# Kernel tuning notes

Hardware: AMD Instinct MI355X
Metric: run time of the kernel (lower is better)

The kernel has to match this reference:

```python
import jax, jax.numpy as jnp
import numpy as np

DIM = 128
HEADS = 4
WIN = 7
N = WIN * WIN  # 49 tokens per window
B = 64         # images
BDIM = 64      # windows per image (56/7)^2
B_ = B * BDIM  # 4096 total windows
HEAD_DIM = DIM // HEADS
SCALE = HEAD_DIM ** (-0.5)


def _rel_index():
    ch, cw = np.meshgrid(np.arange(WIN), np.arange(WIN), indexing='ij')
    coords = np.stack([ch.ravel(), cw.ravel()])            # [2, N]
    rel = coords[:, :, None] - coords[:, None, :]          # [2, N, N]
    rel = rel.transpose(1, 2, 0).astype(np.int32)
    rel[:, :, 0] += WIN - 1
    rel[:, :, 1] += WIN - 1
    rel[:, :, 0] *= 2 * WIN - 1
    return jnp.asarray(rel.sum(-1))                        # [N, N] in [0, 169)


def setup_inputs() -> dict:
    key = jax.random.key(0)
    ks = jax.random.split(key, 7)
    return {
        'x': jax.random.normal(ks[0], (B_, N, DIM), jnp.float32),
        'q_global': jax.random.normal(ks[1], (B, 1, HEADS, N, HEAD_DIM), jnp.float32),
        'rel_bias_table': jax.random.normal(ks[2], (169, HEADS), jnp.float32) * 0.02,
        'W_kv': jax.random.normal(ks[3], (DIM, 2 * DIM), jnp.float32) / np.sqrt(DIM),
        'b_kv': jnp.zeros((2 * DIM,), jnp.float32),
        'W_proj': jax.random.normal(ks[4], (DIM, DIM), jnp.float32) / np.sqrt(DIM),
        'b_proj': jnp.zeros((DIM,), jnp.float32),
        'rel_index': _rel_index(),
    }


def reference(x, q_global, rel_bias_table, W_kv, b_kv, W_proj, b_proj, rel_index):
    Bw, n, C = x.shape
    Bg = q_global.shape[0]
    bdim = Bw // Bg
    # kv projection: [B_, N, 2, H, hd] -> k, v each [B_, H, N, hd]
    kv = (x @ W_kv + b_kv).reshape(Bw, n, 2, HEADS, HEAD_DIM)
    kv = kv.transpose(2, 0, 3, 1, 4)
    k, v = kv[0], kv[1]
    # broadcast global q over windows of each image
    q = jnp.broadcast_to(q_global, (Bg, bdim, HEADS, n, HEAD_DIM)).reshape(Bw, HEADS, n, HEAD_DIM)
    attn = jnp.einsum('bhnd,bhmd->bhnm', q * SCALE, k)
    bias = rel_bias_table[rel_index]                        # [N, N, H]
    attn = attn + bias.transpose(2, 0, 1)[None]
    attn = jax.nn.softmax(attn, axis=-1)
    out = jnp.einsum('bhnm,bhmd->bhnd', attn, v)
    out = out.transpose(0, 2, 1, 3).reshape(Bw, n, C)
    return out @ W_proj + b_proj
```

## Files before the change

kernel.cpp:

```cpp
#include <hip/hip_runtime.h>

#define SCALE 0.17677669529663687f

typedef __attribute__((ext_vector_type(8))) short bf16x8;
typedef __attribute__((ext_vector_type(4))) short bf16x4;
typedef __attribute__((ext_vector_type(4))) float f32x4;

__device__ inline short cvt_bf16(float f) {
    union { float f; unsigned u; } v; v.f = f;
    unsigned r = v.u + 0x7fffu + ((v.u >> 16) & 1u);
    return (short)(r >> 16);
}
__device__ inline short cvt_bf16_fast(float f) {
    union { float f; unsigned u; } v; v.f = f;
    return (short)((v.u + 0x8000u) >> 16);
}
__device__ inline unsigned pack_bf16x2(float f0, float f1) {
    union { float f; unsigned u; } a, b; a.f = f0; b.f = f1;
    return __builtin_amdgcn_perm(b.u + 0x8000u, a.u + 0x8000u, 0x07060302u);
}

#if __has_builtin(__builtin_amdgcn_mfma_f32_16x16x16bf16_1k)
__device__ inline f32x4 mfma16x16(bf16x4 a, bf16x4 b, f32x4 c) {
    return __builtin_amdgcn_mfma_f32_16x16x16bf16_1k(a, b, c, 0, 0, 0);
}
#else
__device__ inline f32x4 mfma16x16(bf16x4 a, bf16x4 b, f32x4 c) {
    asm("v_mfma_f32_16x16x16_bf16 %0, %1, %2, %0" : "+v"(c) : "v"(a), "v"(b));
    return c;
}
#endif

#define WS_WPT  32768
#define WS_QW   49152
#define WS_BIAS 450560

__global__ void prep_kernel(const float* __restrict__ qg,
                            const float* __restrict__ rbt,
                            const float* __restrict__ wkv,
                            const float* __restrict__ wpj,
                            const int*   __restrict__ ridx,
                            short* __restrict__ ws) {
    int i = blockIdx.x * 256 + threadIdx.x;
    if (i < 32768) {
        int k = i >> 8, c = i & 255;
        ws[c * 128 + k] = cvt_bf16(wkv[i]);
        return;
    }
    i -= 32768;
    if (i < 16384) {
        int k = i >> 7, c = i & 127;
        ws[WS_WPT + c * 128 + k] = cvt_bf16(wpj[i]);
        return;
    }
    i -= 16384;
    if (i < 100352) {
        float4 q4 = *(const float4*)(qg + (long)i * 4);
        unsigned lo = (unsigned)(unsigned short)cvt_bf16(q4.x * SCALE) |
                      ((unsigned)(unsigned short)cvt_bf16(q4.y * SCALE) << 16);
        unsigned hi = (unsigned)(unsigned short)cvt_bf16(q4.z * SCALE) |
                      ((unsigned)(unsigned short)cvt_bf16(q4.w * SCALE) << 16);
        uint2 u; u.x = lo; u.y = hi;
        *(uint2*)(ws + WS_QW + (long)i * 4) = u;
        return;
    }
    i -= 100352;
    if (i < 12544) {
        int h = i / 3136, rem = i % 3136, ir = rem >> 6, j = rem & 63;
        float* bias = (float*)(ws + WS_BIAS);
        bias[i] = (j < 49) ? rbt[ridx[ir * 49 + j] * 4 + h] : -3.0e38f;
    }
}

#define KOFF    6664
#define KSLOT   1960
#define SMEM_SZ 14504

__global__ __launch_bounds__(256, 4) void win_attn_kernel(
        const float* __restrict__ x,
        const short* __restrict__ ws,
        const float* __restrict__ bkv,
        const float* __restrict__ bpj,
        float* __restrict__ out) {
    const int b    = blockIdx.x;
    const int img  = b >> 6;
    const int tid  = threadIdx.x;
    const int w    = tid >> 6;
    const int lane = tid & 63;
    const int quad = lane >> 4;
    const int l16  = lane & 15;

    const short* wkvt  = ws;
    const short* wpt   = ws + WS_WPT;
    const short* qw    = ws + WS_QW;
    const float* biasb = (const float*)(ws + WS_BIAS);

    __shared__ __align__(16) short smem[SMEM_SZ];
    short* xs = smem;
    short* os = smem;

    const f32x4 fzero = {0.f, 0.f, 0.f, 0.f};
    const int h = w;

    const float* xb = x + (long)b * 49 * 128;
    #pragma unroll
    for (int it = 0; it < 4; ++it) {
        int chunk = tid + it * 256;
        if (chunk < 784) {
            int row = chunk >> 4, c8 = (chunk & 15) * 8;
            const float* p = xb + row * 128 + c8;
            float4 a = *(const float4*)p;
            float4 c = *(const float4*)(p + 4);
            union { uint4 u; bf16x8 v; } pk;
            pk.u.x = pack_bf16x2(a.x, a.y);
            pk.u.y = pack_bf16x2(a.z, a.w);
            pk.u.z = pack_bf16x2(c.x, c.y);
            pk.u.w = pack_bf16x2(c.z, c.w);
            *(bf16x8*)(xs + row * 136 + c8) = pk.v;
        }
    }
    bf16x8 bfrk[4][2];
    #pragma unroll
    for (int kk = 0; kk < 4; ++kk)
        #pragma unroll
        for (int nt = 0; nt < 2; ++nt)
            bfrk[kk][nt] = *(const bf16x8*)(wkvt + (h * 32 + nt * 16 + l16) * 128 + kk * 32 + quad * 8);
    __syncthreads();

    short* ksl = smem + KOFF + h * KSLOT;
    {
        f32x4 acck[2][4];
        #pragma unroll
        for (int nt = 0; nt < 2; ++nt)
            #pragma unroll
            for (int mi = 0; mi < 4; ++mi) acck[nt][mi] = fzero;

        __builtin_amdgcn_s_setprio(1);
        #pragma unroll
        for (int kk = 0; kk < 4; ++kk) {
            #pragma unroll
            for (int mi = 0; mi < 4; ++mi) {
                int tok = mi * 16 + l16; if (tok > 48) tok = 48;
                bf16x8 af = *(const bf16x8*)(xs + tok * 136 + kk * 32 + quad * 8);
                #pragma unroll
                for (int nt = 0; nt < 2; ++nt)
                    acck[nt][mi] = __builtin_amdgcn_mfma_f32_16x16x32_bf16(af, bfrk[kk][nt], acck[nt][mi], 0, 0, 0);
            }
        }
        __builtin_amdgcn_s_setprio(0);
        #pragma unroll
        for (int nt = 0; nt < 2; ++nt) {
            const int d = nt * 16 + l16;
            const float bv = bkv[h * 32 + d];
            short* kdst = ksl + d;
            #pragma unroll
            for (int mi = 0; mi < 4; ++mi)
                #pragma unroll
                for (int r = 0; r < 4; ++r) {
                    int tok = mi * 16 + quad * 4 + r;
                    if (tok < 49) kdst[tok * 40] = cvt_bf16_fast(acck[nt][mi][r] + bv);
                }
        }
    }

    bf16x4 vfrag[2][4];
    {
        f32x4 accv[2][4];
        #pragma unroll
        for (int nv = 0; nv < 2; ++nv)
            #pragma unroll
            for (int mi = 0; mi < 4; ++mi) accv[nv][mi] = fzero;

        __builtin_amdgcn_s_setprio(1);
        #pragma unroll
        for (int kk = 0; kk < 4; ++kk) {
            bf16x8 bfr[2];
            #pragma unroll
            for (int nv = 0; nv < 2; ++nv)
                bfr[nv] = *(const bf16x8*)(wkvt + (128 + h * 32 + nv * 16 + l16) * 128 + kk * 32 + quad * 8);
            #pragma unroll
            for (int mi = 0; mi < 4; ++mi) {
                int tok = mi * 16 + l16; if (tok > 48) tok = 48;
                bf16x8 af = *(const bf16x8*)(xs + tok * 136 + kk * 32 + quad * 8);
                #pragma unroll
                for (int nv = 0; nv < 2; ++nv)
                    accv[nv][mi] = __builtin_amdgcn_mfma_f32_16x16x32_bf16(af, bfr[nv], accv[nv][mi], 0, 0, 0);
            }
        }
        __builtin_amdgcn_s_setprio(0);
        #pragma unroll
        for (int nv = 0; nv < 2; ++nv) {
            const float bv = bkv[128 + h * 32 + nv * 16 + l16];
            #pragma unroll
            for (int kt = 0; kt < 4; ++kt) {
                union { unsigned u[2]; bf16x4 v; } pk;
                pk.u[0] = pack_bf16x2(accv[nv][kt][0] + bv, accv[nv][kt][1] + bv);
                pk.u[1] = pack_bf16x2(accv[nv][kt][2] + bv, accv[nv][kt][3] + bv);
                vfrag[nv][kt] = pk.v;
            }
        }
    }

    const short* qh = qw + (long)(img * 4 + h) * 49 * 32;
    bf16x8 qfr[4];
    #pragma unroll
    for (int ni = 0; ni < 4; ++ni) {
        int ic = ni * 16 + l16; if (ic > 48) ic = 48;
        qfr[ni] = *(const bf16x8*)(qh + ic * 32 + quad * 8);
    }
    bf16x8 kfr[4];
    #pragma unroll
    for (int mi = 0; mi < 4; ++mi) {
        int kr = mi * 16 + l16; if (kr > 48) kr = 48;
        kfr[mi] = *(const bf16x8*)(ksl + kr * 40 + quad * 8);
    }

    f32x4 oacc[4][2];
    #pragma unroll
    for (int mo = 0; mo < 4; ++mo)
        #pragma unroll
        for (int nv = 0; nv < 2; ++nv) oacc[mo][nv] = fzero;

    #pragma unroll
    for (int ni = 0; ni < 4; ++ni) {
        f32x4 sacc[4] = {fzero, fzero, fzero, fzero};
        __builtin_amdgcn_s_setprio(1);
        #pragma unroll
        for (int mi = 0; mi < 4; ++mi)
            sacc[mi] = __builtin_amdgcn_mfma_f32_16x16x32_bf16(kfr[mi], qfr[ni], sacc[mi], 0, 0, 0);
        __builtin_amdgcn_s_setprio(0);

        int ic = ni * 16 + l16; if (ic > 48) ic = 48;
        const float* bp = biasb + (h * 49 + ic) * 64;
        #pragma unroll
        for (int mi = 0; mi < 4; ++mi) {
            float4 b4 = *(const float4*)(bp + mi * 16 + quad * 4);
            sacc[mi][0] += b4.x; sacc[mi][1] += b4.y;
            sacc[mi][2] += b4.z; sacc[mi][3] += b4.w;
        }
        float mm[4];
        #pragma unroll
        for (int mi = 0; mi < 4; ++mi)
            mm[mi] = fmaxf(fmaxf(fmaxf(sacc[mi][0], sacc[mi][1]), sacc[mi][2]), sacc[mi][3]);
        float m = fmaxf(fmaxf(mm[0], mm[1]), fmaxf(mm[2], mm[3]));
        m = fmaxf(m, __shfl_xor(m, 16, 64));
        m = fmaxf(m, __shfl_xor(m, 32, 64));
        float ps[4];
        #pragma unroll
        for (int mi = 0; mi < 4; ++mi) {
            float e0 = __expf(sacc[mi][0] - m);
            float e1 = __expf(sacc[mi][1] - m);
            float e2 = __expf(sacc[mi][2] - m);
            float e3 = __expf(sacc[mi][3] - m);
            sacc[mi][0] = e0; sacc[mi][1] = e1; sacc[mi][2] = e2; sacc[mi][3] = e3;
            ps[mi] = (e0 + e1) + (e2 + e3);
        }
        float sum = (ps[0] + ps[1]) + (ps[2] + ps[3]);
        sum += __shfl_xor(sum, 16, 64);
        sum += __shfl_xor(sum, 32, 64);
        float inv = 1.0f / sum;
        __builtin_amdgcn_s_setprio(1);
        #pragma unroll
        for (int kt = 0; kt < 4; ++kt) {
            union { unsigned u[2]; bf16x4 v; } pk;
            pk.u[0] = pack_bf16x2(sacc[kt][0] * inv, sacc[kt][1] * inv);
            pk.u[1] = pack_bf16x2(sacc[kt][2] * inv, sacc[kt][3] * inv);
            #pragma unroll
            for (int nv = 0; nv < 2; ++nv)
                oacc[ni][nv] = mfma16x16(pk.v, vfrag[nv][kt], oacc[ni][nv]);
        }
        __builtin_amdgcn_s_setprio(0);
    }

    bf16x8 wfragA[4][2];
    #pragma unroll
    for (int kk = 0; kk < 4; ++kk)
        #pragma unroll
        for (int ct = 0; ct < 2; ++ct)
            wfragA[kk][ct] = *(const bf16x8*)(wpt + ((w * 2 + ct) * 16 + l16) * 128 + kk * 32 + quad * 8);

    __syncthreads();

    #pragma unroll
    for (int mo = 0; mo < 4; ++mo)
        #pragma unroll
        for (int nv = 0; nv < 2; ++nv)
            #pragma unroll
            for (int r = 0; r < 4; ++r) {
                int tok = mo * 16 + quad * 4 + r;
                os[tok * 136 + h * 32 + nv * 16 + l16] = cvt_bf16_fast(oacc[mo][nv][r]);
            }
    __syncthreads();

    f32x4 pacc[2][4];
    #pragma unroll
    for (int ct = 0; ct < 2; ++ct)
        #pragma unroll
        for (int mi = 0; mi < 4; ++mi) pacc[ct][mi] = fzero;
    __builtin_amdgcn_s_setprio(1);
    #pragma unroll
    for (int kk = 0; kk < 4; ++kk) {
        bf16x8 ofrag[4];
        #pragma unroll
        for (int mi = 0; mi < 4; ++mi)
            ofrag[mi] = *(const bf16x8*)(os + (mi * 16 + l16) * 136 + kk * 32 + quad * 8);
        #pragma unroll
        for (int ct = 0; ct < 2; ++ct)
            #pragma unroll
            for (int mi = 0; mi < 4; ++mi)
                pacc[ct][mi] = __builtin_amdgcn_mfma_f32_16x16x32_bf16(ofrag[mi], wfragA[kk][ct], pacc[ct][mi], 0, 0, 0);
    }
    __builtin_amdgcn_s_setprio(0);
    #pragma unroll
    for (int ct = 0; ct < 2; ++ct) {
        const int c0 = (w * 2 + ct) * 16;
        const float bb = bpj[c0 + l16];
        #pragma unroll
        for (int mi = 0; mi < 4; ++mi)
            #pragma unroll
            for (int r = 0; r < 4; ++r) {
                int tok = mi * 16 + quad * 4 + r;
                if (tok < 49)
                    out[((long)b * 49 + tok) * 128 + c0 + l16] = pacc[ct][mi][r] + bb;
            }
    }
}

extern "C" void kernel_launch(void* const* d_in, const int* in_sizes, int n_in,
                              void* d_out, int out_size, void* d_ws, size_t ws_size,
                              hipStream_t stream) {
    const float* x    = (const float*)d_in[0];
    const float* qg   = (const float*)d_in[1];
    const float* rbt  = (const float*)d_in[2];
    const float* wkv  = (const float*)d_in[3];
    const float* bkv  = (const float*)d_in[4];
    const float* wpj  = (const float*)d_in[5];
    const float* bpj  = (const float*)d_in[6];
    const int*   ridx = (const int*)d_in[7];
    short* ws = (short*)d_ws;

    const int prep_total = 32768 + 16384 + 100352 + 12544;
    prep_kernel<<<(prep_total + 255) / 256, 256, 0, stream>>>(qg, rbt, wkv, wpj, ridx, ws);
    win_attn_kernel<<<4096, 256, 0, stream>>>(x, ws, bkv, bpj, (float*)d_out);
}
```

Before: 267.3 us.

## Make attention kernel persistent over four windows with x prefetch and exp-bias softmax

The grid drops from 4096 to 1024 blocks, and each block loops over four windows. The next window's x is loaded into registers while the current attention runs, then packed into shared memory after the barrier. The output staging buffer moves to the K region so the x buffer can be refilled. Softmax precomputes exp(bias) in the prep kernel and multiplies it in, dropping the max subtraction and max reductions; this risks overflow when scores are large, and adds register pressure from the prefetch buffers.

```diff
diff --git a/kernel.cpp b/kernel.cpp
--- a/kernel.cpp
+++ b/kernel.cpp
@@ -67,8 +67,8 @@
     i -= 100352;
     if (i < 12544) {
         int h = i / 3136, rem = i % 3136, ir = rem >> 6, j = rem & 63;
-        float* bias = (float*)(ws + WS_BIAS);
-        bias[i] = (j < 49) ? rbt[ridx[ir * 49 + j] * 4 + h] : -3.0e38f;
+        float* eb = (float*)(ws + WS_BIAS);
+        eb[i] = (j < 49) ? __expf(rbt[ridx[ir * 49 + j] * 4 + h]) : 0.f;
     }
 }
 
@@ -82,247 +82,272 @@
         const float* __restrict__ bkv,
         const float* __restrict__ bpj,
         float* __restrict__ out) {
-    const int b    = blockIdx.x;
-    const int img  = b >> 6;
+    const int b0   = blockIdx.x;
     const int tid  = threadIdx.x;
     const int w    = tid >> 6;
     const int lane = tid & 63;
     const int quad = lane >> 4;
     const int l16  = lane & 15;
-
-    const short* wkvt  = ws;
-    const short* wpt   = ws + WS_WPT;
-    const short* qw    = ws + WS_QW;
-    const float* biasb = (const float*)(ws + WS_BIAS);
+    const int h    = w;
+
+    const short* wkvt = ws;
+    const short* wpt  = ws + WS_WPT;
+    const short* qw   = ws + WS_QW;
+    const float* ebb  = (const float*)(ws + WS_BIAS);
 
     __shared__ __align__(16) short smem[SMEM_SZ];
-    short* xs = smem;
-    short* os = smem;
+    short* xs  = smem;
+    short* os  = smem + KOFF;
+    short* ksl = smem + KOFF + h * KSLOT;
 
     const f32x4 fzero = {0.f, 0.f, 0.f, 0.f};
-    const int h = w;
-
-    const float* xb = x + (long)b * 49 * 128;
-    #pragma unroll
+
+    {
+        const float* xb = x + (long)b0 * 49 * 128;
+        #pragma unroll
+        for (int it4 = 0; it4 < 4; ++it4) {
+            int chunk = tid + it4 * 256;
+            if (chunk < 784) {
+                int row = chunk >> 4, c8 = (chunk & 15) * 8;
+                const float* p = xb + row * 128 + c8;
+                float4 a = *(const float4*)p;
+                float4 c = *(const float4*)(p + 4);
+                union { uint4 u; bf16x8 v; } pk;
+                pk.u.x = pack_bf16x2(a.x, a.y);
+                pk.u.y = pack_bf16x2(a.z, a.w);
+                pk.u.z = pack_bf16x2(c.x, c.y);
+                pk.u.w = pack_bf16x2(c.z, c.w);
+                *(bf16x8*)(xs + row * 136 + c8) = pk.v;
+            }
+        }
+    }
+
     for (int it = 0; it < 4; ++it) {
-        int chunk = tid + it * 256;
-        if (chunk < 784) {
-            int row = chunk >> 4, c8 = (chunk & 15) * 8;
-            const float* p = xb + row * 128 + c8;
-            float4 a = *(const float4*)p;
-            float4 c = *(const float4*)(p + 4);
-            union { uint4 u; bf16x8 v; } pk;
-            pk.u.x = pack_bf16x2(a.x, a.y);
-            pk.u.y = pack_bf16x2(a.z, a.w);
-            pk.u.z = pack_bf16x2(c.x, c.y);
-            pk.u.w = pack_bf16x2(c.z, c.w);
-            *(bf16x8*)(xs + row * 136 + c8) = pk.v;
-        }
-    }
-    bf16x8 bfrk[4][2];
-    #pragma unroll
-    for (int kk = 0; kk < 4; ++kk)
-        #pragma unroll
-        for (int nt = 0; nt < 2; ++nt)
-            bfrk[kk][nt] = *(const bf16x8*)(wkvt + (h * 32 + nt * 16 + l16) * 128 + kk * 32 + quad * 8);
-    __syncthreads();
-
-    short* ksl = smem + KOFF + h * KSLOT;
-    {
-        f32x4 acck[2][4];
-        #pragma unroll
-        for (int nt = 0; nt < 2; ++nt)
-            #pragma unroll
-            for (int mi = 0; mi < 4; ++mi) acck[nt][mi] = fzero;
-
-        __builtin_amdgcn_s_setprio(1);
-        #pragma unroll
-        for (int kk = 0; kk < 4; ++kk) {
+        const int b   = it * 1024 + b0;
+        const int img = b >> 6;
+        __syncthreads();
+
+        {
+            f32x4 acck[2][4];
+            #pragma unroll
+            for (int nt = 0; nt < 2; ++nt)
+                #pragma unroll
+                for (int mi = 0; mi < 4; ++mi) acck[nt][mi] = fzero;
+
+            __builtin_amdgcn_s_setprio(1);
+            #pragma unroll
+            for (int kk = 0; kk < 4; ++kk) {
+                bf16x8 bfr[2];
+                #pragma unroll
+                for (int nt = 0; nt < 2; ++nt)
+                    bfr[nt] = *(const bf16x8*)(wkvt + (h * 32 + nt * 16 + l16) * 128 + kk * 32 + quad * 8);
+                #pragma unroll
+                for (int mi = 0; mi < 4; ++mi) {
+                    int tok = mi * 16 + l16; if (tok > 48) tok = 48;
+                    bf16x8 af = *(const bf16x8*)(xs + tok * 136 + kk * 32 + quad * 8);
+                    #pragma unroll
+                    for (int nt = 0; nt < 2; ++nt)
+                        acck[nt][mi] = __builtin_amdgcn_mfma_f32_16x16x32_bf16(af, bfr[nt], acck[nt][mi], 0, 0, 0);
+                }
+            }
+            __builtin_amdgcn_s_setprio(0);
+            #pragma unroll
+            for (int nt = 0; nt < 2; ++nt) {
+                const int d = nt * 16 + l16;
+                const float bv = bkv[h * 32 + d];
+                short* kdst = ksl + d;
+                #pragma unroll
+                for (int mi = 0; mi < 3; ++mi)
+                    #pragma unroll
+                    for (int r = 0; r < 4; ++r)
+                        kdst[(mi * 16 + quad * 4 + r) * 40] = cvt_bf16_fast(acck[nt][mi][r] + bv);
+                if (quad == 0)
+                    kdst[48 * 40] = cvt_bf16_fast(acck[nt][3][0] + bv);
+            }
+        }
+
+        bf16x4 vfrag[2][4];
+        {
+            f32x4 accv[2][4];
+            #pragma unroll
+            for (int nv = 0; nv < 2; ++nv)
+                #pragma unroll
+                for (int mi = 0; mi < 4; ++mi) accv[nv][mi] = fzero;
+
+            __builtin_amdgcn_s_setprio(1);
+            #pragma unroll
+            for (int kk = 0; kk < 4; ++kk) {
+                bf16x8 bfr[2];
+                #pragma unroll
+                for (int nv = 0; nv < 2; ++nv)
+                    bfr[nv] = *(const bf16x8*)(wkvt + (128 + h * 32 + nv * 16 + l16) * 128 + kk * 32 + quad * 8);
+                #pragma unroll
+                for (int mi = 0; mi < 4; ++mi) {
+                    int tok = mi * 16 + l16; if (tok > 48) tok = 48;
+                    bf16x8 af = *(const bf16x8*)(xs + tok * 136 + kk * 32 + quad * 8);
+                    #pragma unroll
+                    for (int nv = 0; nv < 2; ++nv)
+                        accv[nv][mi] = __builtin_amdgcn_mfma_f32_16x16x32_bf16(af, bfr[nv], accv[nv][mi], 0, 0, 0);
+                }
+            }
+            __builtin_amdgcn_s_setprio(0);
+            #pragma unroll
+            for (int nv = 0; nv < 2; ++nv) {
+                const float bv = bkv[128 + h * 32 + nv * 16 + l16];
+                #pragma unroll
+                for (int kt = 0; kt < 4; ++kt) {
+                    union { unsigned u[2]; bf16x4 v; } pk;
+                    pk.u[0] = pack_bf16x2(accv[nv][kt][0] + bv, accv[nv][kt][1] + bv);
+                    pk.u[1] = pack_bf16x2(accv[nv][kt][2] + bv, accv[nv][kt][3] + bv);
+                    vfrag[nv][kt] = pk.v;
+                }
+            }
+        }
+
+        const short* qh = qw + (long)(img * 4 + h) * 49 * 32;
+        bf16x8 qfr[4];
+        #pragma unroll
+        for (int ni = 0; ni < 4; ++ni) {
+            int ic = ni * 16 + l16; if (ic > 48) ic = 48;
+            qfr[ni] = *(const bf16x8*)(qh + ic * 32 + quad * 8);
+        }
+        bf16x8 kfr[4];
+        #pragma unroll
+        for (int mi = 0; mi < 4; ++mi) {
+            int kr = mi * 16 + l16; if (kr > 48) kr = 48;
+            kfr[mi] = *(const bf16x8*)(ksl + kr * 40 + quad * 8);
+        }
+
+        f32x4 oacc[4][2];
+        #pragma unroll
+        for (int mo = 0; mo < 4; ++mo)
+            #pragma unroll
+            for (int nv = 0; nv < 2; ++nv) oacc[mo][nv] = fzero;
+
+        #pragma unroll
+        for (int ni = 0; ni < 4; ++ni) {
+            f32x4 sacc[4] = {fzero, fzero, fzero, fzero};
+            __builtin_amdgcn_s_setprio(1);
+            #pragma unroll
+            for (int mi = 0; mi < 4; ++mi)
+                sacc[mi] = __builtin_amdgcn_mfma_f32_16x16x32_bf16(kfr[mi], qfr[ni], sacc[mi], 0, 0, 0);
+            __builtin_amdgcn_s_setprio(0);
+
+            int ic = ni * 16 + l16; if (ic > 48) ic = 48;
+            const float* bp = ebb + (h * 49 + ic) * 64;
+            float4 e4[4];
+            #pragma unroll
+            for (int mi = 0; mi < 4; ++mi)
+                e4[mi] = *(const float4*)(bp + mi * 16 + quad * 4);
+
+            float ps[4];
             #pragma unroll
             for (int mi = 0; mi < 4; ++mi) {
-                int tok = mi * 16 + l16; if (tok > 48) tok = 48;
-                bf16x8 af = *(const bf16x8*)(xs + tok * 136 + kk * 32 + quad * 8);
-                #pragma unroll
-                for (int nt = 0; nt < 2; ++nt)
-                    acck[nt][mi] = __builtin_amdgcn_mfma_f32_16x16x32_bf16(af, bfrk[kk][nt], acck[nt][mi], 0, 0, 0);
-            }
-        }
-        __builtin_amdgcn_s_setprio(0);
-        #pragma unroll
-        for (int nt = 0; nt < 2; ++nt) {
-            const int d = nt * 16 + l16;
-            const float bv = bkv[h * 32 + d];
-            short* kdst = ksl + d;
-            #pragma unroll
-            for (int mi = 0; mi < 4; ++mi)
-                #pragma unroll
-                for (int r = 0; r < 4; ++r) {
-                    int tok = mi * 16 + quad * 4 + r;
-                    if (tok < 49) kdst[tok * 40] = cvt_bf16_fast(acck[nt][mi][r] + bv);
-                }
-        }
-    }
-
-    bf16x4 vfrag[2][4];
-    {
-        f32x4 accv[2][4];
-        #pragma unroll
-        for (int nv = 0; nv < 2; ++nv)
-            #pragma unroll
-            for (int mi = 0; mi < 4; ++mi) accv[nv][mi] = fzero;
-
-        __builtin_amdgcn_s_setprio(1);
-        #pragma unroll
-        for (int kk = 0; kk < 4; ++kk) {
-            bf16x8 bfr[2];
-            #pragma unroll
-            for (int nv = 0; nv < 2; ++nv)
-                bfr[nv] = *(const bf16x8*)(wkvt + (128 + h * 32 + nv * 16 + l16) * 128 + kk * 32 + quad * 8);
-            #pragma unroll
-            for (int mi = 0; mi < 4; ++mi) {
-                int tok = mi * 16 + l16; if (tok > 48) tok = 48;
-                bf16x8 af = *(const bf16x8*)(xs + tok * 136 + kk * 32 + quad * 8);
-                #pragma unroll
-                for (int nv = 0; nv < 2; ++nv)
-                    accv[nv][mi] = __builtin_amdgcn_mfma_f32_16x16x32_bf16(af, bfr[nv], accv[nv][mi], 0, 0, 0);
-            }
-        }
-        __builtin_amdgcn_s_setprio(0);
-        #pragma unroll
-        for (int nv = 0; nv < 2; ++nv) {
-            const float bv = bkv[128 + h * 32 + nv * 16 + l16];
+                float p0 = __expf(sacc[mi][0]) * e4[mi].x;
+                float p1 = __expf(sacc[mi][1]) * e4[mi].y;
+                float p2 = __expf(sacc[mi][2]) * e4[mi].z;
+                float p3 = __expf(sacc[mi][3]) * e4[mi].w;
+                sacc[mi][0] = p0; sacc[mi][1] = p1; sacc[mi][2] = p2; sacc[mi][3] = p3;
+                ps[mi] = (p0 + p1) + (p2 + p3);
+            }
+            float sum = (ps[0] + ps[1]) + (ps[2] + ps[3]);
+            sum += __shfl_xor(sum, 16, 64);
+            sum += __shfl_xor(sum, 32, 64);
+            float inv = 1.0f / sum;
+
+            __builtin_amdgcn_s_setprio(1);
             #pragma unroll
             for (int kt = 0; kt < 4; ++kt) {
                 union { unsigned u[2]; bf16x4 v; } pk;
-                pk.u[0] = pack_bf16x2(accv[nv][kt][0] + bv, accv[nv][kt][1] + bv);
-                pk.u[1] = pack_bf16x2(accv[nv][kt][2] + bv, accv[nv][kt][3] + bv);
-                vfrag[nv][kt] = pk.v;
-            }
-        }
-    }
-
-    const short* qh = qw + (long)(img * 4 + h) * 49 * 32;
-    bf16x8 qfr[4];
-    #pragma unroll
-    for (int ni = 0; ni < 4; ++ni) {
-        int ic = ni * 16 + l16; if (ic > 48) ic = 48;
-        qfr[ni] = *(const bf16x8*)(qh + ic * 32 + quad * 8);
-    }
-    bf16x8 kfr[4];
-    #pragma unroll
-    for (int mi = 0; mi < 4; ++mi) {
-        int kr = mi * 16 + l16; if (kr > 48) kr = 48;
-        kfr[mi] = *(const bf16x8*)(ksl + kr * 40 + quad * 8);
-    }
-
-    f32x4 oacc[4][2];
-    #pragma unroll
-    for (int mo = 0; mo < 4; ++mo)
-        #pragma unroll
-        for (int nv = 0; nv < 2; ++nv) oacc[mo][nv] = fzero;
-
-    #pragma unroll
-    for (int ni = 0; ni < 4; ++ni) {
-        f32x4 sacc[4] = {fzero, fzero, fzero, fzero};
+                pk.u[0] = pack_bf16x2(sacc[kt][0] * inv, sacc[kt][1] * inv);
+                pk.u[1] = pack_bf16x2(sacc[kt][2] * inv, sacc[kt][3] * inv);
+                #pragma unroll
+                for (int nv = 0; nv < 2; ++nv)
+                    oacc[ni][nv] = mfma16x16(pk.v, vfrag[nv][kt], oacc[ni][nv]);
+            }
+            __builtin_amdgcn_s_setprio(0);
+        }
+
+        float4 pfa[8], pfb[8];
+        if (it < 3) {
+            const float* xn = x + (long)(b + 1024) * 49 * 128;
+            #pragma unroll
+            for (int it4 = 0; it4 < 4; ++it4) {
+                int chunk = tid + it4 * 256;
+                if (chunk < 784) {
+                    const float* p = xn + (chunk >> 4) * 128 + (chunk & 15) * 8;
+                    pfa[it4] = *(const float4*)p;
+                    pfb[it4] = *(const float4*)(p + 4);
+                }
+            }
+        }
+
+        __syncthreads();
+
+        if (it < 3) {
+            #pragma unroll
+            for (int it4 = 0; it4 < 4; ++it4) {
+                int chunk = tid + it4 * 256;
+                if (chunk < 784) {
+                    union { uint4 u; bf16x8 v; } pk;
+                    pk.u.x = pack_bf16x2(pfa[it4].x, pfa[it4].y);
+                    pk.u.y = pack_bf16x2(pfa[it4].z, pfa[it4].w);
+                    pk.u.z = pack_bf16x2(pfb[it4].x, pfb[it4].y);
+                    pk.u.w = pack_bf16x2(pfb[it4].z, pfb[it4].w);
+                    *(bf16x8*)(xs + (chunk >> 4) * 136 + (chunk & 15) * 8) = pk.v;
+                }
+            }
+        }
+        #pragma unroll
+        for (int mo = 0; mo < 3; ++mo)
+            #pragma unroll
+            for (int nv = 0; nv < 2; ++nv)
+                #pragma unroll
+                for (int r = 0; r < 4; ++r)
+                    os[(mo * 16 + quad * 4 + r) * 136 + h * 32 + nv * 16 + l16] =
+                        cvt_bf16_fast(oacc[mo][nv][r]);
+        if (quad == 0)
+            #pragma unroll
+            for (int nv = 0; nv < 2; ++nv)
+                os[48 * 136 + h * 32 + nv * 16 + l16] = cvt_bf16_fast(oacc[3][nv][0]);
+        __syncthreads();
+
+        f32x4 pacc[2][4];
+        #pragma unroll
+        for (int ct = 0; ct < 2; ++ct)
+            #pragma unroll
+            for (int mi = 0; mi < 4; ++mi) pacc[ct][mi] = fzero;
         __builtin_amdgcn_s_setprio(1);
         #pragma unroll
-        for (int mi = 0; mi < 4; ++mi)
-            sacc[mi] = __builtin_amdgcn_mfma_f32_16x16x32_bf16(kfr[mi], qfr[ni], sacc[mi], 0, 0, 0);
+        for (int kk = 0; kk < 4; ++kk) {
+            bf16x8 ofrag[4];
+            #pragma unroll
+            for (int mi = 0; mi < 4; ++mi) {
+                int row = mi * 16 + l16; if (row > 48) row = 48;
+                ofrag[mi] = *(const bf16x8*)(os + row * 136 + kk * 32 + quad * 8);
+            }
+            #pragma unroll
+            for (int ct = 0; ct < 2; ++ct) {
+                bf16x8 wfrag = *(const bf16x8*)(wpt + ((w * 2 + ct) * 16 + l16) * 128 + kk * 32 + quad * 8);
+                #pragma unroll
+                for (int mi = 0; mi < 4; ++mi)
+                    pacc[ct][mi] = __builtin_amdgcn_mfma_f32_16x16x32_bf16(ofrag[mi], wfrag, pacc[ct][mi], 0, 0, 0);
+            }
+        }
         __builtin_amdgcn_s_setprio(0);
-
-        int ic = ni * 16 + l16; if (ic > 48) ic = 48;
-        const float* bp = biasb + (h * 49 + ic) * 64;
-        #pragma unroll
-        for (int mi = 0; mi < 4; ++mi) {
-            float4 b4 = *(const float4*)(bp + mi * 16 + quad * 4);
-            sacc[mi][0] += b4.x; sacc[mi][1] += b4.y;
-            sacc[mi][2] += b4.z; sacc[mi][3] += b4.w;
-        }
-        float mm[4];
-        #pragma unroll
-        for (int mi = 0; mi < 4; ++mi)
-            mm[mi] = fmaxf(fmaxf(fmaxf(sacc[mi][0], sacc[mi][1]), sacc[mi][2]), sacc[mi][3]);
-        float m = fmaxf(fmaxf(mm[0], mm[1]), fmaxf(mm[2], mm[3]));
-        m = fmaxf(m, __shfl_xor(m, 16, 64));
-        m = fmaxf(m, __shfl_xor(m, 32, 64));
-        float ps[4];
-        #pragma unroll
-        for (int mi = 0; mi < 4; ++mi) {
-            float e0 = __expf(sacc[mi][0] - m);
-            float e1 = __expf(sacc[mi][1] - m);
-            float e2 = __expf(sacc[mi][2] - m);
-            float e3 = __expf(sacc[mi][3] - m);
-            sacc[mi][0] = e0; sacc[mi][1] = e1; sacc[mi][2] = e2; sacc[mi][3] = e3;
-            ps[mi] = (e0 + e1) + (e2 + e3);
-        }
-        float sum = (ps[0] + ps[1]) + (ps[2] + ps[3]);
-        sum += __shfl_xor(sum, 16, 64);
-        sum += __shfl_xor(sum, 32, 64);
-        float inv = 1.0f / sum;
-        __builtin_amdgcn_s_setprio(1);
-        #pragma unroll
-        for (int kt = 0; kt < 4; ++kt) {
-            union { unsigned u[2]; bf16x4 v; } pk;
-            pk.u[0] = pack_bf16x2(sacc[kt][0] * inv, sacc[kt][1] * inv);
-            pk.u[1] = pack_bf16x2(sacc[kt][2] * inv, sacc[kt][3] * inv);
-            #pragma unroll
-            for (int nv = 0; nv < 2; ++nv)
-                oacc[ni][nv] = mfma16x16(pk.v, vfrag[nv][kt], oacc[ni][nv]);
-        }
-        __builtin_amdgcn_s_setprio(0);
-    }
-
-    bf16x8 wfragA[4][2];
-    #pragma unroll
-    for (int kk = 0; kk < 4; ++kk)
-        #pragma unroll
-        for (int ct = 0; ct < 2; ++ct)
-            wfragA[kk][ct] = *(const bf16x8*)(wpt + ((w * 2 + ct) * 16 + l16) * 128 + kk * 32 + quad * 8);
-
-    __syncthreads();
-
-    #pragma unroll
-    for (int mo = 0; mo < 4; ++mo)
-        #pragma unroll
-        for (int nv = 0; nv < 2; ++nv)
-            #pragma unroll
-            for (int r = 0; r < 4; ++r) {
-                int tok = mo * 16 + quad * 4 + r;
-                os[tok * 136 + h * 32 + nv * 16 + l16] = cvt_bf16_fast(oacc[mo][nv][r]);
-            }
-    __syncthreads();
-
-    f32x4 pacc[2][4];
-    #pragma unroll
-    for (int ct = 0; ct < 2; ++ct)
-        #pragma unroll
-        for (int mi = 0; mi < 4; ++mi) pacc[ct][mi] = fzero;
-    __builtin_amdgcn_s_setprio(1);
-    #pragma unroll
-    for (int kk = 0; kk < 4; ++kk) {
-        bf16x8 ofrag[4];
-        #pragma unroll
-        for (int mi = 0; mi < 4; ++mi)
-            ofrag[mi] = *(const bf16x8*)(os + (mi * 16 + l16) * 136 + kk * 32 + quad * 8);
-        #pragma unroll
-        for (int ct = 0; ct < 2; ++ct)
-            #pragma unroll
-            for (int mi = 0; mi < 4; ++mi)
-                pacc[ct][mi] = __builtin_amdgcn_mfma_f32_16x16x32_bf16(ofrag[mi], wfragA[kk][ct], pacc[ct][mi], 0, 0, 0);
-    }
-    __builtin_amdgcn_s_setprio(0);
-    #pragma unroll
-    for (int ct = 0; ct < 2; ++ct) {
-        const int c0 = (w * 2 + ct) * 16;
-        const float bb = bpj[c0 + l16];
-        #pragma unroll
-        for (int mi = 0; mi < 4; ++mi)
-            #pragma unroll
-            for (int r = 0; r < 4; ++r) {
-                int tok = mi * 16 + quad * 4 + r;
-                if (tok < 49)
-                    out[((long)b * 49 + tok) * 128 + c0 + l16] = pacc[ct][mi][r] + bb;
-            }
+        float* outb = out + (long)b * 49 * 128;
+        #pragma unroll
+        for (int ct = 0; ct < 2; ++ct) {
+            const int c0 = (w * 2 + ct) * 16;
+            const float bb = bpj[c0 + l16];
+            #pragma unroll
+            for (int mi = 0; mi < 3; ++mi)
+                #pragma unroll
+                for (int r = 0; r < 4; ++r)
+                    outb[(mi * 16 + quad * 4 + r) * 128 + c0 + l16] = pacc[ct][mi][r] + bb;
+            if (quad == 0)
+                outb[48 * 128 + c0 + l16] = pacc[ct][3][0] + bb;
+        }
     }
 }
 
@@ -341,5 +366,5 @@
 
     const int prep_total = 32768 + 16384 + 100352 + 12544;
     prep_kernel<<<(prep_total + 255) / 256, 256, 0, stream>>>(qg, rbt, wkv, wpj, ridx, ws);
-    win_attn_kernel<<<4096, 256, 0, stream>>>(x, ws, bkv, bpj, (float*)d_out);
-}
+    win_attn_kernel<<<1024, 256, 0, stream>>>(x, ws, bkv, bpj, (float*)d_out);
+}
```

Result: slower. 427.5 us (+60.0%).
